# Kernel optimization log

Measured on AMD Instinct MI355X. Metric: run time of the kernel, lower is better.

Reference implementation:

```python
import jax, jax.numpy as jnp
import numpy as np

HIDDEN = 2048
INTER = 5632
B, S = 2, 2048


def _ternary(key, shape):
    # values in {-1, 0, +1}, matching 2-bit packed ternary weights
    return jax.random.randint(key, shape, -1, 2).astype(jnp.float32)


def setup_inputs() -> dict:
    key = jax.random.key(0)
    ks = jax.random.split(key, 7)
    x = jax.random.normal(ks[0], (B, S, HIDDEN), dtype=jnp.float32)
    gate_w = _ternary(ks[1], (INTER, HIDDEN))   # [intermediate, hidden]
    up_w = _ternary(ks[2], (INTER, HIDDEN))     # [intermediate, hidden]
    down_w = _ternary(ks[3], (HIDDEN, INTER))   # [hidden, intermediate]
    # per-output-channel dequant scales (positive, as from absmean quantization)
    gate_s = jax.random.uniform(ks[4], (INTER,), minval=0.01, maxval=0.1, dtype=jnp.float32)
    up_s = jax.random.uniform(ks[5], (INTER,), minval=0.01, maxval=0.1, dtype=jnp.float32)
    down_s = jax.random.uniform(ks[6], (HIDDEN,), minval=0.01, maxval=0.1, dtype=jnp.float32)
    return {"x": x, "gate_w": gate_w, "up_w": up_w, "down_w": down_w,
            "gate_s": gate_s, "up_s": up_s, "down_s": down_s}


def reference(x, gate_w, up_w, down_w, gate_s, up_s, down_s):
    # x: (B, S, H) -> flatten tokens, as in forward_hidden
    b, s, h = x.shape
    xf = x.reshape(b * s, h)
    # ternary linear = add/sub-only matmul + per-channel scale
    g = jnp.einsum('th,ih->ti', xf, gate_w) * gate_s   # (T, I)
    u = jnp.einsum('th,ih->ti', xf, up_w) * up_s       # (T, I)
    hdn = jax.nn.silu(g) * u                            # gated activation
    out = jnp.einsum('ti,hi->th', hdn, down_w) * down_s  # (T, H)
    return out.reshape(b, s, -1)
```

## Files before the change

kernel.cpp:

```cpp
#include <hip/hip_runtime.h>
#include <stdint.h>
#include <stddef.h>

#define HIDDEN 2048
#define INTER  5632
#define TOKENS 4096
#define BK     64
#define BKI    128

typedef __attribute__((ext_vector_type(8))) _Float16 f16x8;
typedef __attribute__((ext_vector_type(4))) _Float16 f16x4;
typedef __attribute__((ext_vector_type(4))) float    f32x4;
typedef __attribute__((ext_vector_type(4))) int      i32x4;

__device__ __forceinline__ int swz8(int row, int q) {
    return row * 8 + ((q + row) & 7);
}

__global__ __launch_bounds__(256)
void prepass(const float* __restrict__ x,
             const float4* __restrict__ gw, const float4* __restrict__ uw,
             const float4* __restrict__ dw,
             int8_t* __restrict__ xq, float* __restrict__ xs,
             int* __restrict__ go, int* __restrict__ uo,
             f16x4* __restrict__ dno) {
    const int tid = threadIdx.x;
    if (blockIdx.x < TOKENS) {
        const int t = blockIdx.x;
        const float4* row = (const float4*)(x + (size_t)t * HIDDEN);
        float4 v0 = row[tid * 2];
        float4 v1 = row[tid * 2 + 1];
        float m = fmaxf(fmaxf(fabsf(v0.x), fabsf(v0.y)), fmaxf(fabsf(v0.z), fabsf(v0.w)));
        m = fmaxf(m, fmaxf(fmaxf(fabsf(v1.x), fabsf(v1.y)), fmaxf(fabsf(v1.z), fabsf(v1.w))));
        #pragma unroll
        for (int off = 32; off; off >>= 1)
            m = fmaxf(m, __shfl_xor(m, off, 64));
        __shared__ float wmax[4];
        if ((tid & 63) == 0) wmax[tid >> 6] = m;
        __syncthreads();
        m = fmaxf(fmaxf(wmax[0], wmax[1]), fmaxf(wmax[2], wmax[3]));
        m = fmaxf(m, 1e-20f);
        if (tid == 0) xs[t] = m * (1.0f / 127.0f);
        const float inv = 127.0f / m;
        float vals[8] = {v0.x, v0.y, v0.z, v0.w, v1.x, v1.y, v1.z, v1.w};
        int b[8];
        #pragma unroll
        for (int i = 0; i < 8; ++i) b[i] = (int)rintf(vals[i] * inv);
        int lo = (b[0] & 255) | ((b[1] & 255) << 8) | ((b[2] & 255) << 16) | (b[3] << 24);
        int hi = (b[4] & 255) | ((b[5] & 255) << 8) | ((b[6] & 255) << 16) | (b[7] << 24);
        ((int2*)(xq + (size_t)t * HIDDEN))[tid] = make_int2(lo, hi);
        return;
    }
    const int NW4 = INTER * HIDDEN / 4;
    int i = (blockIdx.x - TOKENS) * blockDim.x + tid;
    const int stride = 2048 * blockDim.x;
    for (; i < 3 * NW4; i += stride) {
        if (i < 2 * NW4) {
            const bool is_g = i < NW4;
            const int j = is_g ? i : i - NW4;
            float4 f = is_g ? gw[j] : uw[j];
            int p = ((int)(signed char)(int)f.x & 255)
                  | (((int)(signed char)(int)f.y & 255) << 8)
                  | (((int)(signed char)(int)f.z & 255) << 16)
                  | (((int)(signed char)(int)f.w) << 24);
            if (is_g) go[j] = p; else uo[j] = p;
        } else {
            const int j = i - 2 * NW4;
            float4 f = dw[j];
            f16x4 o;
            o.x = (_Float16)f.x; o.y = (_Float16)f.y;
            o.z = (_Float16)f.z; o.w = (_Float16)f.w;
            dno[j] = o;
        }
    }
}

__global__ __launch_bounds__(256, 2)
void gemm_gateup(const int8_t* __restrict__ Xq,
                 const int8_t* __restrict__ Wg,
                 const int8_t* __restrict__ Wu,
                 const float* __restrict__ xs,
                 const float* __restrict__ gs,
                 const float* __restrict__ us,
                 _Float16* __restrict__ Hm) {
    __shared__ int8_t As [128 * BKI];
    __shared__ int8_t Bgs[128 * BKI];
    __shared__ int8_t Bus[128 * BKI];

    const int pid   = (blockIdx.x % 8) * 176 + blockIdx.x / 8;
    const int local = pid % (16 * 44);
    const int bm    = ((pid / (16 * 44)) * 16 + (local & 15)) * 128;
    const int bn    = (local >> 4) * 128;

    const int tid  = threadIdx.x;
    const int lane = tid & 63;
    const int wave = tid >> 6;
    const int wm   = (wave >> 1) * 64;
    const int wn   = (wave & 1) * 64;
    const int l15  = lane & 15;
    const int lq   = lane >> 4;

    int rowA[4], sgA[4];
    #pragma unroll
    for (int j = 0; j < 4; ++j) {
        const int f = tid + 256 * j;
        rowA[j] = f >> 3;
        sgA[j]  = (((f & 7) - rowA[j]) & 7) * 16;
    }

    i32x4 accg[4][4] = {};
    i32x4 accu[4][4] = {};

    for (int k0 = 0; k0 < HIDDEN; k0 += BKI) {
        #pragma unroll
        for (int j = 0; j < 4; ++j) {
            const int f = tid + 256 * j;
            const int8_t* pX = Xq + (size_t)(bm + rowA[j]) * HIDDEN + k0 + sgA[j];
            const int8_t* pG = Wg + (size_t)(bn + rowA[j]) * HIDDEN + k0 + sgA[j];
            const int8_t* pU = Wu + (size_t)(bn + rowA[j]) * HIDDEN + k0 + sgA[j];
            __builtin_amdgcn_global_load_lds(
                (__attribute__((address_space(1))) void*)pX,
                (__attribute__((address_space(3))) void*)&As[f * 16], 16, 0, 0);
            __builtin_amdgcn_global_load_lds(
                (__attribute__((address_space(1))) void*)pG,
                (__attribute__((address_space(3))) void*)&Bgs[f * 16], 16, 0, 0);
            __builtin_amdgcn_global_load_lds(
                (__attribute__((address_space(1))) void*)pU,
                (__attribute__((address_space(3))) void*)&Bus[f * 16], 16, 0, 0);
        }
        __syncthreads();

        #pragma unroll
        for (int ks = 0; ks < 2; ++ks) {
            const int q = ks * 4 + lq;
            i32x4 a[4];
            #pragma unroll
            for (int im = 0; im < 4; ++im)
                a[im] = *(const i32x4*)&As[swz8(wm + im * 16 + l15, q) * 16];
            #pragma unroll
            for (int jn = 0; jn < 4; ++jn) {
                i32x4 bg = *(const i32x4*)&Bgs[swz8(wn + jn * 16 + l15, q) * 16];
                i32x4 bu = *(const i32x4*)&Bus[swz8(wn + jn * 16 + l15, q) * 16];
                #pragma unroll
                for (int im = 0; im < 4; ++im) {
                    accg[im][jn] = __builtin_amdgcn_mfma_i32_16x16x64_i8(a[im], bg, accg[im][jn], 0, 0, 0);
                    accu[im][jn] = __builtin_amdgcn_mfma_i32_16x16x64_i8(a[im], bu, accu[im][jn], 0, 0, 0);
                }
            }
        }
        __syncthreads();
    }

    #pragma unroll
    for (int jn = 0; jn < 4; ++jn) {
        const int col = bn + wn + jn * 16 + l15;
        const float sg = gs[col];
        const float su = us[col];
        #pragma unroll
        for (int im = 0; im < 4; ++im) {
            const int rbase = bm + wm + im * 16 + lq * 4;
            #pragma unroll
            for (int r = 0; r < 4; ++r) {
                const int row = rbase + r;
                const float st = xs[row];
                float g = (float)accg[im][jn][r] * st * sg;
                float u = (float)accu[im][jn][r] * st * su;
                float h = (g / (1.0f + __expf(-g))) * u;
                Hm[(size_t)row * INTER + col] = (_Float16)h;
            }
        }
    }
}

__global__ __launch_bounds__(256, 2)
void gemm_down(const _Float16* __restrict__ Hm,
               const _Float16* __restrict__ Wd,
               const float* __restrict__ dsc,
               float* __restrict__ out) {
    __shared__ _Float16 As[128 * BK];
    __shared__ _Float16 Bs[128 * BK];

    const int pid = (blockIdx.x % 8) * 64 + blockIdx.x / 8;
    const int loc = pid & 255;
    const int bm  = ((pid >> 8) * 16 + (loc & 15)) * 128;
    const int bn  = (loc >> 4) * 128;

    const int tid  = threadIdx.x;
    const int lane = tid & 63;
    const int wave = tid >> 6;
    const int wm   = (wave >> 1) * 64;
    const int wn   = (wave & 1) * 64;
    const int l15  = lane & 15;
    const int lq   = lane >> 4;

    int rowA[4], sgA[4];
    #pragma unroll
    for (int j = 0; j < 4; ++j) {
        const int f = tid + 256 * j;
        rowA[j] = f >> 3;
        sgA[j]  = (((f & 7) - rowA[j]) & 7) * 8;
    }

    f32x4 acc[4][4] = {};

    for (int k0 = 0; k0 < INTER; k0 += BK) {
        #pragma unroll
        for (int j = 0; j < 4; ++j) {
            const int f = tid + 256 * j;
            const _Float16* pA = Hm + (size_t)(bm + rowA[j]) * INTER + k0 + sgA[j];
            const _Float16* pB = Wd + (size_t)(bn + rowA[j]) * INTER + k0 + sgA[j];
            __builtin_amdgcn_global_load_lds(
                (__attribute__((address_space(1))) void*)pA,
                (__attribute__((address_space(3))) void*)&As[f * 8], 16, 0, 0);
            __builtin_amdgcn_global_load_lds(
                (__attribute__((address_space(1))) void*)pB,
                (__attribute__((address_space(3))) void*)&Bs[f * 8], 16, 0, 0);
        }
        __syncthreads();

        #pragma unroll
        for (int ks = 0; ks < 2; ++ks) {
            const int q = ks * 4 + lq;
            f16x8 a[4];
            #pragma unroll
            for (int im = 0; im < 4; ++im)
                a[im] = *(const f16x8*)&As[swz8(wm + im * 16 + l15, q) * 8];
            #pragma unroll
            for (int jn = 0; jn < 4; ++jn) {
                f16x8 b = *(const f16x8*)&Bs[swz8(wn + jn * 16 + l15, q) * 8];
                #pragma unroll
                for (int im = 0; im < 4; ++im)
                    acc[im][jn] = __builtin_amdgcn_mfma_f32_16x16x32_f16(a[im], b, acc[im][jn], 0, 0, 0);
            }
        }
        __syncthreads();
    }

    #pragma unroll
    for (int jn = 0; jn < 4; ++jn) {
        const int col = bn + wn + jn * 16 + l15;
        const float sd = dsc[col];
        #pragma unroll
        for (int im = 0; im < 4; ++im) {
            const int rbase = bm + wm + im * 16 + lq * 4;
            #pragma unroll
            for (int r = 0; r < 4; ++r)
                out[(size_t)(rbase + r) * HIDDEN + col] = acc[im][jn][r] * sd;
        }
    }
}

extern "C" void kernel_launch(void* const* d_in, const int* in_sizes, int n_in,
                              void* d_out, int out_size, void* d_ws, size_t ws_size,
                              hipStream_t stream) {
    const float* x   = (const float*)d_in[0];
    const float* gw  = (const float*)d_in[1];
    const float* uw  = (const float*)d_in[2];
    const float* dw  = (const float*)d_in[3];
    const float* gsc = (const float*)d_in[4];
    const float* usc = (const float*)d_in[5];
    const float* dsc = (const float*)d_in[6];
    float* out = (float*)d_out;

    char* ws = (char*)d_ws;
    int8_t*   Xq  = (int8_t*)(ws);
    int8_t*   Wg8 = (int8_t*)(ws + 8388608ull);
    int8_t*   Wu8 = (int8_t*)(ws + 19922944ull);
    _Float16* Wdh = (_Float16*)(ws + 31457280ull);
    _Float16* Hm  = (_Float16*)(ws + 54525952ull);
    float*    xs  = (float*)(ws + 100663296ull);

    prepass<<<TOKENS + 2048, 256, 0, stream>>>(
        x, (const float4*)gw, (const float4*)uw, (const float4*)dw,
        Xq, xs, (int*)Wg8, (int*)Wu8, (f16x4*)Wdh);

    gemm_gateup<<<(INTER / 128) * (TOKENS / 128), 256, 0, stream>>>(
        Xq, Wg8, Wu8, xs, gsc, usc, Hm);
    gemm_down<<<(HIDDEN / 128) * (TOKENS / 128), 256, 0, stream>>>(
        Hm, Wdh, dsc, out);
}
```

Baseline: 376.0 us.

## Enlarge gate/up tile to 256 rows with 512 threads and double down-GEMM K step

The gate/up GEMM moves to 512-thread blocks that cover 256 token rows per block and share each loaded gate/up weight tile across twice as many rows, which halves the grid and the weight traffic per token. The down GEMM now processes a K step of 128 per iteration using two 64-wide LDS sub-buffers, so it runs half as many barrier pairs. In exchange, LDS use per block rises and the larger blocks may lower occupancy, and the remapped block-index swizzle changes cache locality.

```diff
diff --git a/kernel.cpp b/kernel.cpp
--- a/kernel.cpp
+++ b/kernel.cpp
@@ -5,7 +5,7 @@
 #define HIDDEN 2048
 #define INTER  5632
 #define TOKENS 4096
-#define BK     64
+#define BKD    128
 #define BKI    128
 
 typedef __attribute__((ext_vector_type(8))) _Float16 f16x8;
@@ -16,6 +16,10 @@
 __device__ __forceinline__ int swz8(int row, int q) {
     return row * 8 + ((q + row) & 7);
 }
+
+#define GLDS16(g, l) __builtin_amdgcn_global_load_lds( \
+    (__attribute__((address_space(1))) void*)(g), \
+    (__attribute__((address_space(3))) void*)(l), 16, 0, 0)
 
 __global__ __launch_bounds__(256)
 void prepass(const float* __restrict__ x,
@@ -75,7 +79,7 @@
     }
 }
 
-__global__ __launch_bounds__(256, 2)
+__global__ __launch_bounds__(512, 2)
 void gemm_gateup(const int8_t* __restrict__ Xq,
                  const int8_t* __restrict__ Wg,
                  const int8_t* __restrict__ Wu,
@@ -83,14 +87,13 @@
                  const float* __restrict__ gs,
                  const float* __restrict__ us,
                  _Float16* __restrict__ Hm) {
-    __shared__ int8_t As [128 * BKI];
+    __shared__ int8_t As [256 * BKI];
     __shared__ int8_t Bgs[128 * BKI];
     __shared__ int8_t Bus[128 * BKI];
 
-    const int pid   = (blockIdx.x % 8) * 176 + blockIdx.x / 8;
-    const int local = pid % (16 * 44);
-    const int bm    = ((pid / (16 * 44)) * 16 + (local & 15)) * 128;
-    const int bn    = (local >> 4) * 128;
+    const int pid = (blockIdx.x % 8) * 88 + blockIdx.x / 8;
+    const int bm  = (pid & 15) * 256;
+    const int bn  = (pid >> 4) * 128;
 
     const int tid  = threadIdx.x;
     const int lane = tid & 63;
@@ -103,30 +106,30 @@
     int rowA[4], sgA[4];
     #pragma unroll
     for (int j = 0; j < 4; ++j) {
-        const int f = tid + 256 * j;
+        const int f = tid + 512 * j;
         rowA[j] = f >> 3;
         sgA[j]  = (((f & 7) - rowA[j]) & 7) * 16;
     }
 
+    const int8_t* gA = Xq + (size_t)bm * HIDDEN;
+    const int8_t* gG = Wg + (size_t)bn * HIDDEN;
+    const int8_t* gU = Wu + (size_t)bn * HIDDEN;
+
     i32x4 accg[4][4] = {};
     i32x4 accu[4][4] = {};
 
     for (int k0 = 0; k0 < HIDDEN; k0 += BKI) {
         #pragma unroll
         for (int j = 0; j < 4; ++j) {
-            const int f = tid + 256 * j;
-            const int8_t* pX = Xq + (size_t)(bm + rowA[j]) * HIDDEN + k0 + sgA[j];
-            const int8_t* pG = Wg + (size_t)(bn + rowA[j]) * HIDDEN + k0 + sgA[j];
-            const int8_t* pU = Wu + (size_t)(bn + rowA[j]) * HIDDEN + k0 + sgA[j];
-            __builtin_amdgcn_global_load_lds(
-                (__attribute__((address_space(1))) void*)pX,
-                (__attribute__((address_space(3))) void*)&As[f * 16], 16, 0, 0);
-            __builtin_amdgcn_global_load_lds(
-                (__attribute__((address_space(1))) void*)pG,
-                (__attribute__((address_space(3))) void*)&Bgs[f * 16], 16, 0, 0);
-            __builtin_amdgcn_global_load_lds(
-                (__attribute__((address_space(1))) void*)pU,
-                (__attribute__((address_space(3))) void*)&Bus[f * 16], 16, 0, 0);
+            const int f = tid + 512 * j;
+            GLDS16(gA + (size_t)rowA[j] * HIDDEN + k0 + sgA[j], &As[f * 16]);
+        }
+        #pragma unroll
+        for (int j = 0; j < 2; ++j) {
+            const int f = tid + 512 * j;
+            const size_t off = (size_t)rowA[j] * HIDDEN + k0 + sgA[j];
+            GLDS16(gG + off, &Bgs[f * 16]);
+            GLDS16(gU + off, &Bus[f * 16]);
         }
         __syncthreads();
 
@@ -177,8 +180,10 @@
                const _Float16* __restrict__ Wd,
                const float* __restrict__ dsc,
                float* __restrict__ out) {
-    __shared__ _Float16 As[128 * BK];
-    __shared__ _Float16 Bs[128 * BK];
+    __shared__ _Float16 As0[128 * 64];
+    __shared__ _Float16 As1[128 * 64];
+    __shared__ _Float16 Bs0[128 * 64];
+    __shared__ _Float16 Bs1[128 * 64];
 
     const int pid = (blockIdx.x % 8) * 64 + blockIdx.x / 8;
     const int loc = pid & 255;
@@ -193,41 +198,44 @@
     const int l15  = lane & 15;
     const int lq   = lane >> 4;
 
-    int rowA[4], sgA[4];
+    int rS[4], sS[4];
     #pragma unroll
     for (int j = 0; j < 4; ++j) {
         const int f = tid + 256 * j;
-        rowA[j] = f >> 3;
-        sgA[j]  = (((f & 7) - rowA[j]) & 7) * 8;
-    }
+        rS[j] = f >> 3;
+        sS[j] = (((f & 7) - (f >> 3)) & 7) * 8;
+    }
+
+    const _Float16* gA = Hm + (size_t)bm * INTER;
+    const _Float16* gB = Wd + (size_t)bn * INTER;
 
     f32x4 acc[4][4] = {};
 
-    for (int k0 = 0; k0 < INTER; k0 += BK) {
+    for (int k0 = 0; k0 < INTER; k0 += BKD) {
         #pragma unroll
         for (int j = 0; j < 4; ++j) {
             const int f = tid + 256 * j;
-            const _Float16* pA = Hm + (size_t)(bm + rowA[j]) * INTER + k0 + sgA[j];
-            const _Float16* pB = Wd + (size_t)(bn + rowA[j]) * INTER + k0 + sgA[j];
-            __builtin_amdgcn_global_load_lds(
-                (__attribute__((address_space(1))) void*)pA,
-                (__attribute__((address_space(3))) void*)&As[f * 8], 16, 0, 0);
-            __builtin_amdgcn_global_load_lds(
-                (__attribute__((address_space(1))) void*)pB,
-                (__attribute__((address_space(3))) void*)&Bs[f * 8], 16, 0, 0);
-        }
-        __syncthreads();
-
-        #pragma unroll
-        for (int ks = 0; ks < 2; ++ks) {
-            const int q = ks * 4 + lq;
+            const size_t oA = (size_t)rS[j] * INTER + k0 + sS[j];
+            GLDS16(gA + oA,      &As0[f * 8]);
+            GLDS16(gA + oA + 64, &As1[f * 8]);
+            const size_t oB = (size_t)rS[j] * INTER + k0 + sS[j];
+            GLDS16(gB + oB,      &Bs0[f * 8]);
+            GLDS16(gB + oB + 64, &Bs1[f * 8]);
+        }
+        __syncthreads();
+
+        #pragma unroll
+        for (int ks = 0; ks < 4; ++ks) {
+            const _Float16* A_ = (ks < 2) ? As0 : As1;
+            const _Float16* B_ = (ks < 2) ? Bs0 : Bs1;
+            const int q = (ks & 1) * 4 + lq;
             f16x8 a[4];
             #pragma unroll
             for (int im = 0; im < 4; ++im)
-                a[im] = *(const f16x8*)&As[swz8(wm + im * 16 + l15, q) * 8];
+                a[im] = *(const f16x8*)&A_[swz8(wm + im * 16 + l15, q) * 8];
             #pragma unroll
             for (int jn = 0; jn < 4; ++jn) {
-                f16x8 b = *(const f16x8*)&Bs[swz8(wn + jn * 16 + l15, q) * 8];
+                f16x8 b = *(const f16x8*)&B_[swz8(wn + jn * 16 + l15, q) * 8];
                 #pragma unroll
                 for (int im = 0; im < 4; ++im)
                     acc[im][jn] = __builtin_amdgcn_mfma_f32_16x16x32_f16(a[im], b, acc[im][jn], 0, 0, 0);
@@ -274,7 +282,7 @@
         x, (const float4*)gw, (const float4*)uw, (const float4*)dw,
         Xq, xs, (int*)Wg8, (int*)Wu8, (f16x4*)Wdh);
 
-    gemm_gateup<<<(INTER / 128) * (TOKENS / 128), 256, 0, stream>>>(
+    gemm_gateup<<<(INTER / 128) * (TOKENS / 256), 512, 0, stream>>>(
         Xq, Wg8, Wu8, xs, gsc, usc, Hm);
     gemm_down<<<(HIDDEN / 128) * (TOKENS / 128), 256, 0, stream>>>(
         Hm, Wdh, dsc, out);
```

Result: slower. 387.2 us (+3.0%).
